# Kernel optimization log

Measured on AMD Instinct MI355X. Metric: run time of the kernel, lower is better.

Reference implementation:

```python
import jax, jax.numpy as jnp
import numpy as np

B, C1, C2, H, W = 4, 128, 256, 128, 128
K, S = 3, 1
N = K * K  # num sampled points = 9
BN_EPS = 1e-5


def setup_inputs() -> dict:
    key = jax.random.key(0)
    ks = jax.random.split(key, 8)
    x = jax.random.normal(ks[0], (B, C1, H, W), jnp.float32)
    # offset-prediction conv: 3x3, stride S, pad 1, out channels 2*N
    w_off = jax.random.normal(ks[1], (2 * N, C1, 3, 3), jnp.float32) * 0.01
    b_off = jnp.zeros((2 * N,), jnp.float32)
    # main conv over the N sampled points: equivalent to Conv2d(C1,C2,(N,1),stride=(N,1),bias=None)
    w_main = jax.random.normal(ks[2], (C2, C1, N), jnp.float32) * (1.0 / np.sqrt(C1 * N))
    bn_gamma = jax.random.uniform(ks[3], (C2,), jnp.float32, 0.5, 1.5)
    bn_beta = jax.random.normal(ks[4], (C2,), jnp.float32) * 0.1
    bn_mean = jax.random.normal(ks[5], (C2,), jnp.float32) * 0.1
    bn_var = jax.random.uniform(ks[6], (C2,), jnp.float32, 0.5, 1.5)
    return dict(x=x, w_off=w_off, b_off=b_off, w_main=w_main,
                bn_gamma=bn_gamma, bn_beta=bn_beta, bn_mean=bn_mean, bn_var=bn_var)


def _grid_pn():
    # base kernel sampling grid for N points: round(sqrt(N)) x base grid, values 0..base-1
    base = int(round(np.sqrt(N)))
    px, py = np.meshgrid(np.arange(base), np.arange(base), indexing='ij')
    return jnp.asarray(px.reshape(-1), jnp.float32), jnp.asarray(py.reshape(-1), jnp.float32)


def _akconv_forward(x, w_off, b_off, w_main, bn_gamma, bn_beta, bn_mean, bn_var):
    # offset prediction: (b, 2N, h, w)
    offset = jax.lax.conv_general_dilated(
        x, w_off, (S, S), ((1, 1), (1, 1)),
        dimension_numbers=('NCHW', 'OIHW', 'NCHW')) + b_off[None, :, None, None]
    b, _, h, w = offset.shape
    off_x = offset[:, :N].transpose(0, 2, 3, 1)   # (b,h,w,N) row offsets
    off_y = offset[:, N:].transpose(0, 2, 3, 1)   # (b,h,w,N) col offsets
    pn_x, pn_y = _grid_pn()
    p0_x = (jnp.arange(h, dtype=jnp.float32) * S)[None, :, None, None]
    p0_y = (jnp.arange(w, dtype=jnp.float32) * S)[None, None, :, None]
    px = jnp.clip(off_x + pn_x[None, None, None, :] + p0_x, 0.0, H - 1.0)
    py = jnp.clip(off_y + pn_y[None, None, None, :] + p0_y, 0.0, W - 1.0)
    x0 = jnp.clip(jnp.floor(px), 0.0, H - 1.0)
    y0 = jnp.clip(jnp.floor(py), 0.0, W - 1.0)
    x1 = jnp.clip(x0 + 1.0, 0.0, H - 1.0)
    y1 = jnp.clip(y0 + 1.0, 0.0, W - 1.0)
    # bilinear weights (official AKConv formulation)
    g_lt = (1.0 + (x0 - px)) * (1.0 + (y0 - py))
    g_rb = (1.0 - (x1 - px)) * (1.0 - (y1 - py))
    g_lb = (1.0 + (x0 - px)) * (1.0 - (y1 - py))
    g_rt = (1.0 - (x1 - px)) * (1.0 + (y0 - py))
    xf = x.reshape(b, C1, H * W)

    def gather(qx, qy):
        idx = (qx * W + qy).astype(jnp.int32).reshape(b, 1, h * w * N)
        g = jnp.take_along_axis(xf, jnp.broadcast_to(idx, (b, C1, h * w * N)), axis=2)
        return g.reshape(b, C1, h, w, N)

    # fused bilinear combine: (b, C1, h, w, N)
    x_off = (g_lt[:, None] * gather(x0, y0)
             + g_rb[:, None] * gather(x1, y1)
             + g_lb[:, None] * gather(x0, y1)
             + g_rt[:, None] * gather(x1, y0))
    # main conv over sampled points == Conv2d(kernel=(N,1), stride=(N,1)) on rearranged tensor
    out = jnp.einsum('bchwn,ocn->bohw', x_off, w_main)
    # inference-mode BatchNorm
    inv = bn_gamma / jnp.sqrt(bn_var + BN_EPS)
    out = out * inv[None, :, None, None] + (bn_beta - bn_mean * inv)[None, :, None, None]
    # wrapper SiLU activation
    return jax.nn.silu(out)


def reference(x, w_off, b_off, w_main, bn_gamma, bn_beta, bn_mean, bn_var):
    return _akconv_forward(x, w_off, b_off, w_main, bn_gamma, bn_beta, bn_mean, bn_var)
```

## Files before the change

kernel.cpp:

```cpp
#include <hip/hip_runtime.h>
#include <math.h>

typedef __attribute__((ext_vector_type(8))) short short8;
typedef __attribute__((ext_vector_type(4))) float f32x4;

#define BB  4
#define C1  128
#define C2  256
#define HH  128
#define WW  128
#define NPT 9
#define HWN (HH*WW)

#define XT_OFF    0ull
#define WB3_OFF   16777216ull
#define WOF32_OFF (WB3_OFF + 589824ull)
#define BN_OFF    (WOF32_OFF + 82944ull)
#define OFFP_OFF  (BN_OFF + 2048ull)

__device__ __forceinline__ ushort f2bf(float f) {
  uint u = __builtin_bit_cast(uint, f);
  u += 0x7FFFu + ((u >> 16) & 1u);
  return (ushort)(u >> 16);
}
__device__ __forceinline__ float bf2f(ushort u) {
  return __builtin_bit_cast(float, ((uint)u) << 16);
}

__global__ __launch_bounds__(256) void prep(
    const float* __restrict__ w_main, const float* __restrict__ w_off,
    const float* __restrict__ g, const float* __restrict__ be,
    const float* __restrict__ mu, const float* __restrict__ var,
    ushort* ws_u, float* ws_f) {
  int t = blockIdx.x * 256 + threadIdx.x;
  if (t < C1 * NPT * C2) {
    int j = t & 7, lane = (t >> 3) & 63, kc = (t >> 9) & 3;
    int ob = (t >> 11) & 15, n = t >> 15;
    int o = ob * 16 + (lane & 15);
    int c = kc * 32 + (lane >> 4) * 8 + j;
    ws_u[WB3_OFF / 2 + t] = f2bf(w_main[(o * C1 + c) * NPT + n]);
  } else if (t < C1 * NPT * C2 + 128 * 2 * 81) {
    int e = t - C1 * NPT * C2;
    int c2 = e / 81, r81 = e - c2 * 81;
    int q = c2 & 1, c = c2 >> 1;
    int tap = r81 / 9, i = r81 - tap * 9;
    int oc = q * 9 + i;
    ws_f[WOF32_OFF / 4 + e] = w_off[(oc * C1 + c) * 9 + tap];
  } else if (t < C1 * NPT * C2 + 128 * 2 * 81 + C2) {
    int o = t - (C1 * NPT * C2 + 128 * 2 * 81);
    float inv = g[o] * rsqrtf(var[o] + 1e-5f);
    ws_f[BN_OFF / 4 + o] = inv;
    ws_f[BN_OFF / 4 + 256 + o] = be[o] - mu[o] * inv;
  }
}

__global__ __launch_bounds__(256) void transpose_x(
    const float* __restrict__ x, ushort* ws_u) {
  __shared__ __align__(16) ushort tile[32][68];
  int bid = blockIdx.x;
  int wt = bid & 1, h = (bid >> 1) & 127, cb = (bid >> 8) & 3, b = bid >> 10;
  int c0 = cb * 32, w0 = wt * 64;
  int tid = threadIdx.x;
  int wl = tid & 63, rr = tid >> 6;
#pragma unroll
  for (int it = 0; it < 8; ++it) {
    int ci = it * 4 + rr;
    tile[ci][wl] = f2bf(x[(((size_t)b * C1 + c0 + ci) * HWN) + h * WW + w0 + wl]);
  }
  __syncthreads();
  int wl2 = tid >> 2, cg = tid & 3;
  short8 pk;
#pragma unroll
  for (int k = 0; k < 8; ++k) pk[k] = (short)tile[cg * 8 + k][wl2];
  *(short8*)(ws_u + XT_OFF / 2 +
             (((size_t)(b * HH + h) * WW + w0 + wl2) * C1 + c0 + cg * 8)) = pk;
}

__global__ __launch_bounds__(256) void off_conv_part(
    const float* __restrict__ x, const float* __restrict__ b_off,
    const float* __restrict__ ws_f, float* __restrict__ part) {
  int blk = blockIdx.x;
  int cg = blk & 3, bh = blk >> 2;
  int h = bh & 127, b = bh >> 7;
  int tid = threadIdx.x;
  int w = tid & 127, q = tid >> 7;
  int qu = __builtin_amdgcn_readfirstlane(q);
  const float* wq = ws_f + WOF32_OFF / 4 + qu * 81;
  const float* xb = x + ((size_t)b * C1 + cg * 32) * HWN;

  float acc[9];
#pragma unroll
  for (int i = 0; i < 9; ++i) acc[i] = (cg == 0) ? b_off[qu * 9 + i] : 0.f;

  int hc0 = (h >= 1) ? h - 1 : 0, hc2 = (h < 127) ? h + 1 : 127;
  int wc0 = (w >= 1) ? w - 1 : 0, wc2 = (w < 127) ? w + 1 : 127;
  bool vh0 = (h >= 1), vh2 = (h < 127);
  bool vw0 = (w >= 1), vw2 = (w < 127);
  int o[9];
  o[0] = hc0 * 128 + wc0; o[1] = hc0 * 128 + w; o[2] = hc0 * 128 + wc2;
  o[3] = h   * 128 + wc0; o[4] = h   * 128 + w; o[5] = h   * 128 + wc2;
  o[6] = hc2 * 128 + wc0; o[7] = hc2 * 128 + w; o[8] = hc2 * 128 + wc2;
  bool vm[9];
  vm[0] = vh0 && vw0; vm[1] = vh0; vm[2] = vh0 && vw2;
  vm[3] = vw0;        vm[4] = true; vm[5] = vw2;
  vm[6] = vh2 && vw0; vm[7] = vh2; vm[8] = vh2 && vw2;

  for (int ci = 0; ci < 32; ++ci) {
    const float* xc = xb + (size_t)ci * HWN;
    float xv[9];
#pragma unroll
    for (int k = 0; k < 9; ++k) {
      float r = xc[o[k]];
      xv[k] = vm[k] ? r : 0.f;
    }
    const float* wp = wq + (cg * 32 + ci) * 162;
#pragma unroll
    for (int tap = 0; tap < 9; ++tap)
#pragma unroll
      for (int i = 0; i < 9; ++i)
        acc[i] = fmaf(xv[tap], wp[tap * 9 + i], acc[i]);
  }
  int pos = (b * HH + h) * WW + w;
  float* pd = part + ((size_t)cg * 65536 + pos) * 20 + qu * 9;
#pragma unroll
  for (int i = 0; i < 9; ++i) pd[i] = acc[i];
}

__global__ __launch_bounds__(256) void off_reduce(
    const float* __restrict__ part, float* __restrict__ ws_f) {
  int e = blockIdx.x * 256 + threadIdx.x;
  if (e >= 65536 * 18) return;
  int pos = e / 18, oc = e - pos * 18;
  size_t i0 = (size_t)pos * 20 + oc;
  float s = part[i0]
          + part[i0 + (size_t)65536 * 20]
          + part[i0 + (size_t)2 * 65536 * 20]
          + part[i0 + (size_t)3 * 65536 * 20];
  ws_f[OFFP_OFF / 4 + i0] = s;
}

#define ALDS_STRIDE 136
__global__ __launch_bounds__(512) void akconv_main_mfma8(
    const ushort* ws_u, const float* ws_f, float* out) {
  __shared__ ushort sxy[576];
  __shared__ __align__(16) f32x4 swgt[576];
  __shared__ __align__(16) ushort alds[2][64 * ALDS_STRIDE];

  int tid = threadIdx.x;
  int blk = blockIdx.x;
  int xcd = blk & 7, idx = blk >> 3;
  int b  = xcd >> 1;
  int h  = ((xcd & 1) << 6) + (idx >> 1);
  int wt = idx & 1;
  int w0 = wt * 64;
  const float* offp = ws_f + OFFP_OFF / 4;

  for (int t = tid; t < 576; t += 512) {
    int n = t >> 6, wl = t & 63;
    int pos = (b * HH + h) * WW + w0 + wl;
    float ox = offp[pos * 20 + n];
    float oy = offp[pos * 20 + 9 + n];
    float px = ox + (float)(n / 3) + (float)h;
    float py = oy + (float)(n - (n / 3) * 3) + (float)(w0 + wl);
    px = fminf(fmaxf(px, 0.f), 127.f);
    py = fminf(fmaxf(py, 0.f), 127.f);
    float x0 = floorf(px), y0 = floorf(py);
    float x1 = fminf(x0 + 1.f, 127.f), y1 = fminf(y0 + 1.f, 127.f);
    f32x4 g;
    g[0] = (1.f + (x0 - px)) * (1.f + (y0 - py));
    g[1] = (1.f - (x1 - px)) * (1.f - (y1 - py));
    g[2] = (1.f + (x0 - px)) * (1.f - (y1 - py));
    g[3] = (1.f - (x1 - px)) * (1.f + (y0 - py));
    sxy[t] = (ushort)(((int)x0 << 8) | (int)y0);
    swgt[t] = g;
  }

  const char* xTb = (const char*)ws_u + (size_t)b * (HWN * 256);
  const ushort* wB3 = ws_u + WB3_OFF / 2;
  int lane = tid & 63, r = lane & 15, kg = lane >> 4;
  int obu = __builtin_amdgcn_readfirstlane(tid >> 6) * 2;

  int p0  = tid >> 4;
  int p1  = p0 + 32;
  int oct = tid & 15;
  int coff = oct * 16;
  int wr0 = p0 * ALDS_STRIDE + oct * 8;
  int wr1 = p1 * ALDS_STRIDE + oct * 8;

  f32x4 acc[4][2];
#pragma unroll
  for (int mi = 0; mi < 4; ++mi)
#pragma unroll
    for (int oi = 0; oi < 2; ++oi) acc[mi][oi] = (f32x4)0.0f;

  __syncthreads();

  short8 gv[2][4];
  f32x4 gw0, gw1;

#define GLOAD(nn)                                                       \
  {                                                                     \
    int e0 = sxy[(nn) * 64 + p0];                                       \
    int e1 = sxy[(nn) * 64 + p1];                                       \
    gw0 = swgt[(nn) * 64 + p0];                                         \
    gw1 = swgt[(nn) * 64 + p1];                                         \
    int ax0 = e0 >> 8, ay0 = e0 & 255;                                  \
    int ax1 = min(ax0 + 1, 127), ay1 = min(ay0 + 1, 127);               \
    int bx0 = e1 >> 8, by0 = e1 & 255;                                  \
    int bx1 = min(bx0 + 1, 127), by1 = min(by0 + 1, 127);               \
    gv[0][0] = *(const short8*)(xTb + (ax0 << 15) + (ay0 << 8) + coff); \
    gv[0][1] = *(const short8*)(xTb + (ax1 << 15) + (ay1 << 8) + coff); \
    gv[0][2] = *(const short8*)(xTb + (ax0 << 15) + (ay1 << 8) + coff); \
    gv[0][3] = *(const short8*)(xTb + (ax1 << 15) + (ay0 << 8) + coff); \
    gv[1][0] = *(const short8*)(xTb + (bx0 << 15) + (by0 << 8) + coff); \
    gv[1][1] = *(const short8*)(xTb + (bx1 << 15) + (by1 << 8) + coff); \
    gv[1][2] = *(const short8*)(xTb + (bx0 << 15) + (by1 << 8) + coff); \
    gv[1][3] = *(const short8*)(xTb + (bx1 << 15) + (by0 << 8) + coff); \
  }

#define GCOMBINE(bufb)                                                  \
  {                                                                     \
    short8 pk0, pk1;                                                    \
    _Pragma("unroll")                                                   \
    for (int j = 0; j < 8; ++j) {                                       \
      float f0 = gw0[0] * bf2f((ushort)gv[0][0][j])                     \
               + gw0[1] * bf2f((ushort)gv[0][1][j])                     \
               + gw0[2] * bf2f((ushort)gv[0][2][j])                     \
               + gw0[3] * bf2f((ushort)gv[0][3][j]);                    \
      float f1 = gw1[0] * bf2f((ushort)gv[1][0][j])                     \
               + gw1[1] * bf2f((ushort)gv[1][1][j])                     \
               + gw1[2] * bf2f((ushort)gv[1][2][j])                     \
               + gw1[3] * bf2f((ushort)gv[1][3][j]);                    \
      pk0[j] = (short)f2bf(f0);                                         \
      pk1[j] = (short)f2bf(f1);                                         \
    }                                                                   \
    *(short8*)(&alds[bufb][wr0]) = pk0;                                 \
    *(short8*)(&alds[bufb][wr1]) = pk1;                                 \
  }

  GLOAD(0);
  GCOMBINE(0);
  __syncthreads();

  for (int n = 0; n < 9; ++n) {
    int buf = n & 1;
    if (n < 8) GLOAD(n + 1);
#pragma unroll
    for (int kc = 0; kc < 4; ++kc) {
      short8 b0 = *(const short8*)(wB3 + ((((size_t)(n * 16 + obu) * 4 + kc) * 64 + lane) * 8));
      short8 b1 = *(const short8*)(wB3 + ((((size_t)(n * 16 + obu + 1) * 4 + kc) * 64 + lane) * 8));
#pragma unroll
      for (int mi = 0; mi < 4; ++mi) {
        short8 a = *(const short8*)(&alds[buf][(mi * 16 + r) * ALDS_STRIDE + (kc * 4 + kg) * 8]);
        acc[mi][0] = __builtin_amdgcn_mfma_f32_16x16x32_bf16(b0, a, acc[mi][0], 0, 0, 0);
        acc[mi][1] = __builtin_amdgcn_mfma_f32_16x16x32_bf16(b1, a, acc[mi][1], 0, 0, 0);
      }
    }
    if (n < 8) GCOMBINE(buf ^ 1);
    __syncthreads();
  }
#undef GLOAD
#undef GCOMBINE

  const float* bnA = ws_f + BN_OFF / 4;
  const float* bnB = bnA + 256;
  int owu = obu * 16;
#pragma unroll
  for (int oi = 0; oi < 2; ++oi) {
#pragma unroll
    for (int mi = 0; mi < 4; ++mi) {
#pragma unroll
      for (int j = 0; j < 4; ++j) {
        int o = owu + oi * 16 + kg * 4 + j;
        float sA = bnA[o], sB = bnB[o];
        float v = acc[mi][oi][j] * sA + sB;
        float sv = v / (1.f + __expf(-v));
        out[(((size_t)b * C2 + o) * HWN) + h * WW + w0 + mi * 16 + r] = sv;
      }
    }
  }
}

extern "C" void kernel_launch(void* const* d_in, const int* in_sizes, int n_in,
                              void* d_out, int out_size, void* d_ws, size_t ws_size,
                              hipStream_t stream) {
  const float* x        = (const float*)d_in[0];
  const float* w_off    = (const float*)d_in[1];
  const float* b_off    = (const float*)d_in[2];
  const float* w_main   = (const float*)d_in[3];
  const float* bn_gamma = (const float*)d_in[4];
  const float* bn_beta  = (const float*)d_in[5];
  const float* bn_mean  = (const float*)d_in[6];
  const float* bn_var   = (const float*)d_in[7];
  ushort* ws_u = (ushort*)d_ws;
  float*  ws_f = (float*)d_ws;
  float*  out  = (float*)d_out;

  int prep_tasks = C1 * NPT * C2 + 128 * 2 * 81 + C2;
  prep<<<(prep_tasks + 255) / 256, 256, 0, stream>>>(
      w_main, w_off, bn_gamma, bn_beta, bn_mean, bn_var, ws_u, ws_f);
  transpose_x<<<BB * 4 * HH * 2, 256, 0, stream>>>(x, ws_u);
  off_conv_part<<<4 * BB * HH, 256, 0, stream>>>(x, b_off, ws_f, out);
  off_reduce<<<(65536 * 18 + 255) / 256, 256, 0, stream>>>(out, ws_f);
  akconv_main_mfma8<<<BB * HH * 2, 512, 0, stream>>>(ws_u, ws_f, out);
}
```

Measured before the change: 153.4 us.

## Drop offset-conv split-K reduce, widen main kernel to 1024 threads, pack bf16 conversion

The offset conv now runs over all 128 input channels in a single block per row. Its results go straight into a channel-planar offset buffer, which removes the partial-sum pass and the separate reduce kernel. The main kernel grows to 16 waves of 1024 threads, each handling one output-channel group with a single gather point per thread, so registers per thread drop. The bilinear combine now uses bit masks and v_cvt_pk_bf16_f32 packing. The trade-off is that the offset conv has 4x fewer blocks with longer serial loops, and the larger blocks may limit occupancy.

```diff
diff --git a/kernel.cpp b/kernel.cpp
--- a/kernel.cpp
+++ b/kernel.cpp
@@ -3,6 +3,7 @@
 
 typedef __attribute__((ext_vector_type(8))) short short8;
 typedef __attribute__((ext_vector_type(4))) float f32x4;
+typedef __attribute__((ext_vector_type(4))) uint  uint4v;
 
 #define BB  4
 #define C1  128
@@ -23,8 +24,8 @@
   u += 0x7FFFu + ((u >> 16) & 1u);
   return (ushort)(u >> 16);
 }
-__device__ __forceinline__ float bf2f(ushort u) {
-  return __builtin_bit_cast(float, ((uint)u) << 16);
+__device__ __forceinline__ float u2f(uint u) {
+  return __builtin_bit_cast(float, u);
 }
 
 __global__ __launch_bounds__(256) void prep(
@@ -76,21 +77,21 @@
              (((size_t)(b * HH + h) * WW + w0 + wl2) * C1 + c0 + cg * 8)) = pk;
 }
 
-__global__ __launch_bounds__(256) void off_conv_part(
+__global__ __launch_bounds__(256) void off_conv_f32b(
     const float* __restrict__ x, const float* __restrict__ b_off,
-    const float* __restrict__ ws_f, float* __restrict__ part) {
-  int blk = blockIdx.x;
-  int cg = blk & 3, bh = blk >> 2;
-  int h = bh & 127, b = bh >> 7;
+    float* ws_f) {
+  int bid = blockIdx.x;
+  int h = bid & 127, b = bid >> 7;
   int tid = threadIdx.x;
   int w = tid & 127, q = tid >> 7;
   int qu = __builtin_amdgcn_readfirstlane(q);
   const float* wq = ws_f + WOF32_OFF / 4 + qu * 81;
-  const float* xb = x + ((size_t)b * C1 + cg * 32) * HWN;
+  const float* xb = x + (size_t)b * C1 * HWN;
+  float* offp = ws_f + OFFP_OFF / 4;
 
   float acc[9];
 #pragma unroll
-  for (int i = 0; i < 9; ++i) acc[i] = (cg == 0) ? b_off[qu * 9 + i] : 0.f;
+  for (int i = 0; i < 9; ++i) acc[i] = b_off[qu * 9 + i];
 
   int hc0 = (h >= 1) ? h - 1 : 0, hc2 = (h < 127) ? h + 1 : 127;
   int wc0 = (w >= 1) ? w - 1 : 0, wc2 = (w < 127) ? w + 1 : 127;
@@ -105,15 +106,15 @@
   vm[3] = vw0;        vm[4] = true; vm[5] = vw2;
   vm[6] = vh2 && vw0; vm[7] = vh2; vm[8] = vh2 && vw2;
 
-  for (int ci = 0; ci < 32; ++ci) {
-    const float* xc = xb + (size_t)ci * HWN;
+  for (int c = 0; c < C1; ++c) {
+    const float* xc = xb + (size_t)c * HWN;
     float xv[9];
 #pragma unroll
     for (int k = 0; k < 9; ++k) {
-      float r = xc[o[k]];
-      xv[k] = vm[k] ? r : 0.f;
+      float rr = xc[o[k]];
+      xv[k] = vm[k] ? rr : 0.f;
     }
-    const float* wp = wq + (cg * 32 + ci) * 162;
+    const float* wp = wq + c * 162;
 #pragma unroll
     for (int tap = 0; tap < 9; ++tap)
 #pragma unroll
@@ -121,26 +122,13 @@
         acc[i] = fmaf(xv[tap], wp[tap * 9 + i], acc[i]);
   }
   int pos = (b * HH + h) * WW + w;
-  float* pd = part + ((size_t)cg * 65536 + pos) * 20 + qu * 9;
-#pragma unroll
-  for (int i = 0; i < 9; ++i) pd[i] = acc[i];
-}
-
-__global__ __launch_bounds__(256) void off_reduce(
-    const float* __restrict__ part, float* __restrict__ ws_f) {
-  int e = blockIdx.x * 256 + threadIdx.x;
-  if (e >= 65536 * 18) return;
-  int pos = e / 18, oc = e - pos * 18;
-  size_t i0 = (size_t)pos * 20 + oc;
-  float s = part[i0]
-          + part[i0 + (size_t)65536 * 20]
-          + part[i0 + (size_t)2 * 65536 * 20]
-          + part[i0 + (size_t)3 * 65536 * 20];
-  ws_f[OFFP_OFF / 4 + i0] = s;
+#pragma unroll
+  for (int i = 0; i < 9; ++i)
+    offp[(size_t)(qu * 9 + i) * 65536 + pos] = acc[i];
 }
 
 #define ALDS_STRIDE 136
-__global__ __launch_bounds__(512) void akconv_main_mfma8(
+__global__ __launch_bounds__(1024, 8) void akconv_main_mfma16(
     const ushort* ws_u, const float* ws_f, float* out) {
   __shared__ ushort sxy[576];
   __shared__ __align__(16) f32x4 swgt[576];
@@ -155,11 +143,11 @@
   int w0 = wt * 64;
   const float* offp = ws_f + OFFP_OFF / 4;
 
-  for (int t = tid; t < 576; t += 512) {
-    int n = t >> 6, wl = t & 63;
+  if (tid < 576) {
+    int n = tid >> 6, wl = tid & 63;
     int pos = (b * HH + h) * WW + w0 + wl;
-    float ox = offp[pos * 20 + n];
-    float oy = offp[pos * 20 + 9 + n];
+    float ox = offp[(size_t)n * 65536 + pos];
+    float oy = offp[(size_t)(9 + n) * 65536 + pos];
     float px = ox + (float)(n / 3) + (float)h;
     float py = oy + (float)(n - (n / 3) * 3) + (float)(w0 + wl);
     px = fminf(fmaxf(px, 0.f), 127.f);
@@ -171,71 +159,62 @@
     g[1] = (1.f - (x1 - px)) * (1.f - (y1 - py));
     g[2] = (1.f + (x0 - px)) * (1.f - (y1 - py));
     g[3] = (1.f - (x1 - px)) * (1.f + (y0 - py));
-    sxy[t] = (ushort)(((int)x0 << 8) | (int)y0);
-    swgt[t] = g;
+    sxy[tid] = (ushort)(((int)x0 << 8) | (int)y0);
+    swgt[tid] = g;
   }
 
   const char* xTb = (const char*)ws_u + (size_t)b * (HWN * 256);
   const ushort* wB3 = ws_u + WB3_OFF / 2;
   int lane = tid & 63, r = lane & 15, kg = lane >> 4;
-  int obu = __builtin_amdgcn_readfirstlane(tid >> 6) * 2;
-
-  int p0  = tid >> 4;
-  int p1  = p0 + 32;
+  int wv = __builtin_amdgcn_readfirstlane(tid >> 6);
+
+  int p   = tid >> 4;
   int oct = tid & 15;
   int coff = oct * 16;
-  int wr0 = p0 * ALDS_STRIDE + oct * 8;
-  int wr1 = p1 * ALDS_STRIDE + oct * 8;
-
-  f32x4 acc[4][2];
-#pragma unroll
-  for (int mi = 0; mi < 4; ++mi)
-#pragma unroll
-    for (int oi = 0; oi < 2; ++oi) acc[mi][oi] = (f32x4)0.0f;
+  int wr = p * ALDS_STRIDE + oct * 8;
+
+  f32x4 acc[4];
+#pragma unroll
+  for (int mi = 0; mi < 4; ++mi) acc[mi] = (f32x4)0.0f;
 
   __syncthreads();
 
-  short8 gv[2][4];
-  f32x4 gw0, gw1;
+  short8 gv[4];
+  f32x4 gw;
 
 #define GLOAD(nn)                                                       \
   {                                                                     \
-    int e0 = sxy[(nn) * 64 + p0];                                       \
-    int e1 = sxy[(nn) * 64 + p1];                                       \
-    gw0 = swgt[(nn) * 64 + p0];                                         \
-    gw1 = swgt[(nn) * 64 + p1];                                         \
-    int ax0 = e0 >> 8, ay0 = e0 & 255;                                  \
+    int e = (nn) * 64 + p;                                              \
+    int exy = sxy[e];                                                   \
+    gw = swgt[e];                                                       \
+    int ax0 = exy >> 8, ay0 = exy & 255;                                \
     int ax1 = min(ax0 + 1, 127), ay1 = min(ay0 + 1, 127);               \
-    int bx0 = e1 >> 8, by0 = e1 & 255;                                  \
-    int bx1 = min(bx0 + 1, 127), by1 = min(by0 + 1, 127);               \
-    gv[0][0] = *(const short8*)(xTb + (ax0 << 15) + (ay0 << 8) + coff); \
-    gv[0][1] = *(const short8*)(xTb + (ax1 << 15) + (ay1 << 8) + coff); \
-    gv[0][2] = *(const short8*)(xTb + (ax0 << 15) + (ay1 << 8) + coff); \
-    gv[0][3] = *(const short8*)(xTb + (ax1 << 15) + (ay0 << 8) + coff); \
-    gv[1][0] = *(const short8*)(xTb + (bx0 << 15) + (by0 << 8) + coff); \
-    gv[1][1] = *(const short8*)(xTb + (bx1 << 15) + (by1 << 8) + coff); \
-    gv[1][2] = *(const short8*)(xTb + (bx0 << 15) + (by1 << 8) + coff); \
-    gv[1][3] = *(const short8*)(xTb + (bx1 << 15) + (by0 << 8) + coff); \
+    gv[0] = *(const short8*)(xTb + (ax0 << 15) + (ay0 << 8) + coff);    \
+    gv[1] = *(const short8*)(xTb + (ax1 << 15) + (ay1 << 8) + coff);    \
+    gv[2] = *(const short8*)(xTb + (ax0 << 15) + (ay1 << 8) + coff);    \
+    gv[3] = *(const short8*)(xTb + (ax1 << 15) + (ay0 << 8) + coff);    \
   }
 
 #define GCOMBINE(bufb)                                                  \
   {                                                                     \
-    short8 pk0, pk1;                                                    \
+    uint4v g0 = __builtin_bit_cast(uint4v, gv[0]);                      \
+    uint4v g1 = __builtin_bit_cast(uint4v, gv[1]);                      \
+    uint4v g2 = __builtin_bit_cast(uint4v, gv[2]);                      \
+    uint4v pkv;                                                         \
+    uint4v g3 = __builtin_bit_cast(uint4v, gv[3]);                      \
     _Pragma("unroll")                                                   \
-    for (int j = 0; j < 8; ++j) {                                       \
-      float f0 = gw0[0] * bf2f((ushort)gv[0][0][j])                     \
-               + gw0[1] * bf2f((ushort)gv[0][1][j])                     \
-               + gw0[2] * bf2f((ushort)gv[0][2][j])                     \
-               + gw0[3] * bf2f((ushort)gv[0][3][j]);                    \
-      float f1 = gw1[0] * bf2f((ushort)gv[1][0][j])                     \
-               + gw1[1] * bf2f((ushort)gv[1][1][j])                     \
-               + gw1[2] * bf2f((ushort)gv[1][2][j])                     \
-               + gw1[3] * bf2f((ushort)gv[1][3][j]);                    \
-      pk0[j] = (short)f2bf(f0);                                         \
-      pk1[j] = (short)f2bf(f1);                                         \
+    for (int jj = 0; jj < 4; ++jj) {                                    \
+      float flo = gw[0] * u2f(g0[jj] << 16) + gw[1] * u2f(g1[jj] << 16) \
+                + gw[2] * u2f(g2[jj] << 16) + gw[3] * u2f(g3[jj] << 16);\
+      float fhi = gw[0] * u2f(g0[jj] & 0xffff0000u)                     \
+                + gw[1] * u2f(g1[jj] & 0xffff0000u)                     \
+                + gw[2] * u2f(g2[jj] & 0xffff0000u)                     \
+                + gw[3] * u2f(g3[jj] & 0xffff0000u);                    \
+      uint upk;                                                         \
+      asm("v_cvt_pk_bf16_f32 %0, %1, %2" : "=v"(upk) : "v"(flo), "v"(fhi)); \
+      pkv[jj] = upk;                                                    \
     }                                                                   \
-    *(short8*)(&alds[bufb][wr0]) = pk0;                                 \
-    *(short8*)(&alds[bufb][wr1]) = pk1;                                 \
+    *(uint4v*)(&alds[bufb][wr]) = pkv;                                  \
   }
 
   GLOAD(0);
@@ -247,13 +226,12 @@
     if (n < 8) GLOAD(n + 1);
 #pragma unroll
     for (int kc = 0; kc < 4; ++kc) {
-      short8 b0 = *(const short8*)(wB3 + ((((size_t)(n * 16 + obu) * 4 + kc) * 64 + lane) * 8));
-      short8 b1 = *(const short8*)(wB3 + ((((size_t)(n * 16 + obu + 1) * 4 + kc) * 64 + lane) * 8));
+      short8 bfrag = *(const short8*)(wB3 +
+          (((size_t)(n * 16 + wv) * 4 + kc) * 64 + lane) * 8);
 #pragma unroll
       for (int mi = 0; mi < 4; ++mi) {
         short8 a = *(const short8*)(&alds[buf][(mi * 16 + r) * ALDS_STRIDE + (kc * 4 + kg) * 8]);
-        acc[mi][0] = __builtin_amdgcn_mfma_f32_16x16x32_bf16(b0, a, acc[mi][0], 0, 0, 0);
-        acc[mi][1] = __builtin_amdgcn_mfma_f32_16x16x32_bf16(b1, a, acc[mi][1], 0, 0, 0);
+        acc[mi] = __builtin_amdgcn_mfma_f32_16x16x32_bf16(bfrag, a, acc[mi], 0, 0, 0);
       }
     }
     if (n < 8) GCOMBINE(buf ^ 1);
@@ -264,19 +242,16 @@
 
   const float* bnA = ws_f + BN_OFF / 4;
   const float* bnB = bnA + 256;
-  int owu = obu * 16;
-#pragma unroll
-  for (int oi = 0; oi < 2; ++oi) {
+  int ob = wv * 16 + kg * 4;
+#pragma unroll
+  for (int j = 0; j < 4; ++j) {
+    int o = ob + j;
+    float sA = bnA[o], sB = bnB[o];
 #pragma unroll
     for (int mi = 0; mi < 4; ++mi) {
-#pragma unroll
-      for (int j = 0; j < 4; ++j) {
-        int o = owu + oi * 16 + kg * 4 + j;
-        float sA = bnA[o], sB = bnB[o];
-        float v = acc[mi][oi][j] * sA + sB;
-        float sv = v / (1.f + __expf(-v));
-        out[(((size_t)b * C2 + o) * HWN) + h * WW + w0 + mi * 16 + r] = sv;
-      }
+      float v = acc[mi][j] * sA + sB;
+      float sv = v / (1.f + __expf(-v));
+      out[(((size_t)b * C2 + o) * HWN) + h * WW + w0 + mi * 16 + r] = sv;
     }
   }
 }
@@ -300,7 +275,6 @@
   prep<<<(prep_tasks + 255) / 256, 256, 0, stream>>>(
       w_main, w_off, bn_gamma, bn_beta, bn_mean, bn_var, ws_u, ws_f);
   transpose_x<<<BB * 4 * HH * 2, 256, 0, stream>>>(x, ws_u);
-  off_conv_part<<<4 * BB * HH, 256, 0, stream>>>(x, b_off, ws_f, out);
-  off_reduce<<<(65536 * 18 + 255) / 256, 256, 0, stream>>>(out, ws_f);
-  akconv_main_mfma8<<<BB * HH * 2, 512, 0, stream>>>(ws_u, ws_f, out);
-}
+  off_conv_f32b<<<BB * HH, 256, 0, stream>>>(x, b_off, ws_f);
+  akconv_main_mfma16<<<BB * HH * 2, 1024, 0, stream>>>(ws_u, ws_f, out);
+}
```

New measurement: 180.8 us. +17.9%, slower.
